# Kernel optimization log

Measured on AMD Instinct MI355X. Metric: run time of the kernel, lower is better.

Reference implementation:

```python
import jax, jax.numpy as jnp
import numpy as np
from jax import lax

B = 32768  # number of 5x5 patches processed in a batch
NUM_MID = 6  # middle 25->25 conv layers (layers 1..6 of 8)
NUM_W = 6    # predicted kernel weights per pixel


def _conv(x, w, b, pad):
    # x: [B,C,H,W], w: [O,I,kh,kw]
    y = lax.conv_general_dilated(x, w, (1, 1), pad,
                                 dimension_numbers=('NCHW', 'OIHW', 'NCHW'))
    return y + b[None, :, None, None]


def setup_inputs() -> dict:
    key = jax.random.key(0)
    ks = jax.random.split(key, 10)
    s = 0.1
    inp = {
        'input': jax.random.normal(ks[0], (B, 8, 5, 5), dtype=jnp.float32),
        'w0': jax.random.normal(ks[1], (25, 8, 3, 3), dtype=jnp.float32) * s,
        'b0': jax.random.normal(ks[2], (25,), dtype=jnp.float32) * s,
        'wmid': jax.random.normal(ks[3], (NUM_MID, 25, 25, 3, 3), dtype=jnp.float32) * s,
        'bmid': jax.random.normal(ks[4], (NUM_MID, 25), dtype=jnp.float32) * s,
        'wlast': jax.random.normal(ks[5], (NUM_W, 25, 3, 3), dtype=jnp.float32) * s,
        'blast': jax.random.normal(ks[6], (NUM_W,), dtype=jnp.float32) * s,
        'wpost': jax.random.normal(ks[7], (3 * NUM_W, 3, 5, 5), dtype=jnp.float32) * s,
        'bpost': jax.random.normal(ks[8], (3 * NUM_W,), dtype=jnp.float32) * s,
    }
    return inp


def reference(input, w0, b0, wmid, bmid, wlast, blast, wpost, bpost):
    # 8-layer tiny CNN predicting per-pixel softmax weights over NUM_W kernels
    h = jax.nn.relu(_conv(input, w0, b0, 'SAME'))
    for i in range(NUM_MID):  # fixed small layer count
        h = jax.nn.relu(_conv(h, wmid[i], bmid[i], 'SAME'))
    h = _conv(h, wlast, blast, 'SAME')            # [B, NUM_W, 5, 5]
    norm_w = jax.nn.softmax(h, axis=1)            # softmax over weight channels
    # postconv: 5x5 valid conv on first 3 channels -> [B, 3*NUM_W, 1, 1] -> [B,3,NUM_W]
    colors = _conv(input[:, 0:3], wpost, bpost, 'VALID').reshape(B, 3, NUM_W)
    # per-pixel matmul: filtered[:,y,x] = colors @ norm_w[:,y,x]
    filtered = jnp.einsum('bcw,bwyx->bcyx', colors, norm_w)  # [B,3,5,5]
    return filtered
```

## Files before the change

kernel.cpp:

```cpp
#include <hip/hip_runtime.h>
#include <hip/hip_bf16.h>
#include <stdint.h>


typedef short bf16x8 __attribute__((ext_vector_type(8)));
typedef float f32x4  __attribute__((ext_vector_type(4)));

#define WSB_N     73728
#define WSB_EMB   6144
#define WSF_BYTE  147456
#define WSF_BALL  0
#define WSF_BP32  256

#define L_STAGE_STRIDE 136
#define L_INPK   6800
#define L_COLB   12944
#define L_POOL   14096
#define SMB_STRIDE 98

__device__ __forceinline__ float b2f(unsigned short u) {
  union { unsigned int u; float f; } v; v.u = ((unsigned int)u) << 16; return v.f;
}
__device__ __forceinline__ unsigned short f2b(float f) {
  union { float f; unsigned int u; } v; v.f = f;
  unsigned int r = v.u + 0x7fffu + ((v.u >> 16) & 1u);
  return (unsigned short)(r >> 16);
}
__device__ __forceinline__ unsigned int pk2(float lo, float hi) {
  __hip_bfloat162 h = __float22bfloat162_rn(make_float2(lo, hi));
  union { __hip_bfloat162 h; unsigned int u; } v; v.h = h; return v.u;
}
__device__ __forceinline__ bool sniff_is_f32(const void* w0raw) {
  const unsigned short* q = (const unsigned short*)w0raw;
  int hits = 0;
  #pragma unroll
  for (int i = 0; i < 64; ++i) {
    unsigned int e = (q[i] >> 7) & 0xFFu;
    if (e >= 130u) ++hits;
  }
  return hits > 0;
}
__device__ __forceinline__ float ldw(const void* p, long idx, bool f32) {
  return f32 ? ((const float*)p)[idx] : b2f(((const unsigned short*)p)[idx]);
}
__device__ __forceinline__ int kperm(int m) {
  return (m < 16) ? ((m >> 2) * 8 + (m & 3))
                  : (((m - 16) >> 2) * 8 + 4 + (m & 3));
}

__global__ void prep_weights(const void* __restrict__ w0,
                             const void* __restrict__ b0,
                             const void* __restrict__ wm,
                             const void* __restrict__ bm,
                             const void* __restrict__ wl,
                             const void* __restrict__ bl,
                             const void* __restrict__ wp,
                             const void* __restrict__ bp,
                             unsigned short* __restrict__ wsb,
                             float* __restrict__ wsf) {
  const bool f32 = sniff_is_f32(w0);
  int e = blockIdx.x * blockDim.x + threadIdx.x;
  if (e < WSB_N) {
    int l = e / 9216, r = e % 9216, t = r / 1024, r2 = r % 1024;
    int o = r2 >> 5, c = r2 & 31;
    if (l == 7 && o >= 6) return;
    float v = 0.f;
    if (l < 7) {
      int co = kperm(o);
      if (co < 25) {
        if (l == 0) { if (c < 8)  v = ldw(w0, (co * 8 + c) * 9 + t, f32); }
        else        { if (c < 25) v = ldw(wm, (((l - 1) * 25 + co) * 25 + c) * 9 + t, f32); }
      }
    } else {
      if (c < 25) v = ldw(wl, (o * 25 + c) * 9 + t, f32);
    }
    wsb[e] = f2b(v);
  } else if (e < WSB_N + WSB_EMB) {
    int idx = e - WSB_N;
    int hl = idx / 3072, rem = idx % 3072;
    int chunk = rem / 1024, r2 = rem % 1024;
    int o = r2 >> 5, k = r2 & 31;
    float w = (o < 18 && k < 25) ? ldw(wp, (o * 3 + chunk) * 25 + k, f32) : 0.f;
    unsigned short hi = f2b(w);
    unsigned short val = hl ? f2b(w - b2f(hi)) : hi;
    int rowidx = hl * 96 + chunk * 32 + o;
    int t = rowidx / 26, rr = 6 + rowidx % 26;
    wsb[7 * 9216 + t * 1024 + rr * 32 + k] = val;
  } else {
    int q = e - WSB_N - WSB_EMB;
    if (q < 256) {
      int l = q >> 5, m = q & 31;
      float v = 0.f;
      if (l < 7) {
        int co = kperm(m);
        if (co < 25) v = (l == 0) ? ldw(b0, co, f32) : ldw(bm, (l - 1) * 25 + co, f32);
      } else {
        if (m < 6) v = ldw(bl, m, f32);
      }
      wsf[WSF_BALL + q] = v;
    } else if (q < 288) {
      int oc = q - 256;
      wsf[WSF_BP32 + oc] = (oc < 18) ? ldw(bp, oc, f32) : 0.f;
    }
  }
}

__global__ __launch_bounds__(64)
__attribute__((amdgpu_waves_per_eu(2, 2)))
void pcnn_mfma(
    const void* __restrict__ inp,
    const void* __restrict__ w0raw,
    const unsigned short* __restrict__ wsb,
    const float* __restrict__ wsf,
    void* __restrict__ out) {
  __shared__ __align__(16) unsigned char pool[L_POOL];
  short* stage = (short*)pool;
  short* inpk  = (short*)(pool + L_INPK);
  float* colb  = (float*)(pool + L_COLB);
  float* smb   = (float*)pool;

  const bool f32m = sniff_is_f32(w0raw);
  const int lane = threadIdx.x;
  const int col  = lane & 15;
  const int quad = lane >> 4;
  const long g   = blockIdx.x;

  bf16x8 WC[2][3][2];
  #pragma unroll
  for (int hl = 0; hl < 2; ++hl)
    #pragma unroll
    for (int ch = 0; ch < 3; ++ch)
      #pragma unroll
      for (int hf = 0; hf < 2; ++hf) {
        const int rowidx = hl * 96 + ch * 32 + hf * 16 + col;
        const int t = rowidx / 26, rr = 6 + rowidx % 26;
        WC[hl][ch][hf] = *(const bf16x8*)(wsb + 7 * 9216 + t * 1024 + rr * 32 + quad * 8);
      }
  f32x4 c0 = *(const f32x4*)(wsf + WSF_BP32 + quad * 4);
  f32x4 c1 = *(const f32x4*)(wsf + WSF_BP32 + 16 + quad * 4);

  for (int i = lane; i < 672; i += 64) {
    int s = 25 + i % 7, rest = i / 7;
    inpk[rest * 32 + s] = 0;
  }

  #pragma unroll 1
  for (int c0i = 0; c0i < 3200; c0i += 1600) {
    float v[25];
    #pragma unroll
    for (int j = 0; j < 25; ++j)
      v[j] = ldw(inp, g * 3200 + c0i + j * 64 + lane, f32m);
    #pragma unroll
    for (int j = 0; j < 25; ++j) {
      const int e = c0i + j * 64 + lane;
      int b = e / 200, r = e % 200, c = r / 25, px = r % 25;
      unsigned short hi = f2b(v[j]);
      stage[px * L_STAGE_STRIDE + b * 8 + c] = hi;
      if (c < 3) {
        inpk[((0 * 3 + c) * 16 + b) * 32 + px] = hi;
        inpk[((1 * 3 + c) * 16 + b) * 32 + px] = f2b(v[j] - b2f(hi));
      }
    }
  }
  __asm__ volatile("s_waitcnt lgkmcnt(0)" ::: "memory");

  #pragma unroll
  for (int ch = 0; ch < 3; ++ch) {
    bf16x8 Bhi = *(const bf16x8*)(inpk + ((0 * 3 + ch) * 16 + col) * 32 + quad * 8);
    bf16x8 Blo = *(const bf16x8*)(inpk + ((1 * 3 + ch) * 16 + col) * 32 + quad * 8);
    c0 = __builtin_amdgcn_mfma_f32_16x16x32_bf16(WC[0][ch][0], Bhi, c0, 0, 0, 0);
    c0 = __builtin_amdgcn_mfma_f32_16x16x32_bf16(WC[0][ch][0], Blo, c0, 0, 0, 0);
    c0 = __builtin_amdgcn_mfma_f32_16x16x32_bf16(WC[1][ch][0], Bhi, c0, 0, 0, 0);
    c1 = __builtin_amdgcn_mfma_f32_16x16x32_bf16(WC[0][ch][1], Bhi, c1, 0, 0, 0);
    c1 = __builtin_amdgcn_mfma_f32_16x16x32_bf16(WC[0][ch][1], Blo, c1, 0, 0, 0);
    c1 = __builtin_amdgcn_mfma_f32_16x16x32_bf16(WC[1][ch][1], Bhi, c1, 0, 0, 0);
  }
  #pragma unroll
  for (int r = 0; r < 4; ++r) colb[col * 18 + quad * 4 + r] = c0[r];
  if (quad == 0) { colb[col * 18 + 16] = c1[0]; colb[col * 18 + 17] = c1[1]; }

  bf16x8 X[25], Y[25];
  #pragma unroll
  for (int p = 0; p < 25; ++p) {
    union { bf16x8 v; uint4 q4; } t;
    t.q4 = make_uint4(0u, 0u, 0u, 0u);
    if (quad == 0) t.q4 = *(const uint4*)(stage + p * L_STAGE_STRIDE + col * 8);
    X[p] = t.v;
  }

  auto conv = [&](const bf16x8 (&in)[25], bf16x8 (&outp)[25], int l) {
    const unsigned short* WA = wsb + l * 9216;
    bf16x8 A0[9], A1[9];
    #pragma unroll
    for (int t = 0; t < 9; ++t) {
      A0[t] = *(const bf16x8*)(WA + t * 1024 + col * 32 + quad * 8);
      A1[t] = *(const bf16x8*)(WA + t * 1024 + (16 + col) * 32 + quad * 8);
    }
    const f32x4 bias0 = *(const f32x4*)(wsf + WSF_BALL + l * 32 + quad * 4);
    const f32x4 bias1 = *(const f32x4*)(wsf + WSF_BALL + l * 32 + 16 + quad * 4);
    f32x4 p0e, p0o, p1e, p1o;
    #pragma unroll
    for (int p = 0; p < 25; ++p) {
      const int py = p / 5, pxx = p % 5;
      f32x4 a0e = bias0, a1e = bias1;
      f32x4 a0o = {0.f, 0.f, 0.f, 0.f}, a1o = {0.f, 0.f, 0.f, 0.f};
      __builtin_amdgcn_s_setprio(1);
      #pragma unroll
      for (int dy = -1; dy <= 1; ++dy)
        #pragma unroll
        for (int dx = -1; dx <= 1; ++dx)
          if ((unsigned)(py + dy) < 5u && (unsigned)(pxx + dx) < 5u) {
            const int t = (dy + 1) * 3 + (dx + 1);
            const int q = p + dy * 5 + dx;
            if (t & 1) {
              a0o = __builtin_amdgcn_mfma_f32_16x16x32_bf16(A0[t], in[q], a0o, 0, 0, 0);
              a1o = __builtin_amdgcn_mfma_f32_16x16x32_bf16(A1[t], in[q], a1o, 0, 0, 0);
            } else {
              a0e = __builtin_amdgcn_mfma_f32_16x16x32_bf16(A0[t], in[q], a0e, 0, 0, 0);
              a1e = __builtin_amdgcn_mfma_f32_16x16x32_bf16(A1[t], in[q], a1e, 0, 0, 0);
            }
          }
      __builtin_amdgcn_s_setprio(0);
      if (p > 0) {
        union { bf16x8 v; unsigned int uu[4]; } nb;
        nb.uu[0] = pk2(fmaxf(p0e[0] + p0o[0], 0.f), fmaxf(p0e[1] + p0o[1], 0.f));
        nb.uu[1] = pk2(fmaxf(p0e[2] + p0o[2], 0.f), fmaxf(p0e[3] + p0o[3], 0.f));
        nb.uu[2] = pk2(fmaxf(p1e[0] + p1o[0], 0.f), fmaxf(p1e[1] + p1o[1], 0.f));
        nb.uu[3] = pk2(fmaxf(p1e[2] + p1o[2], 0.f), fmaxf(p1e[3] + p1o[3], 0.f));
        outp[p - 1] = nb.v;
      }
      p0e = a0e; p0o = a0o; p1e = a1e; p1o = a1o;
    }
    {
      union { bf16x8 v; unsigned int uu[4]; } nb;
      nb.uu[0] = pk2(fmaxf(p0e[0] + p0o[0], 0.f), fmaxf(p0e[1] + p0o[1], 0.f));
      nb.uu[1] = pk2(fmaxf(p0e[2] + p0o[2], 0.f), fmaxf(p0e[3] + p0o[3], 0.f));
      nb.uu[2] = pk2(fmaxf(p1e[0] + p1o[0], 0.f), fmaxf(p1e[1] + p1o[1], 0.f));
      nb.uu[3] = pk2(fmaxf(p1e[2] + p1o[2], 0.f), fmaxf(p1e[3] + p1o[3], 0.f));
      outp[24] = nb.v;
    }
  };

  conv(X, Y, 0);
  #pragma unroll 1
  for (int i = 0; i < 3; ++i) {
    conv(Y, X, 2 * i + 1);
    conv(X, Y, 2 * i + 2);
  }

  {
    const unsigned short* WA = wsb + 7 * 9216;
    bf16x8 A[9];
    #pragma unroll
    for (int t = 0; t < 9; ++t)
      A[t] = *(const bf16x8*)(WA + t * 1024 + col * 32 + quad * 8);
    const f32x4 biasl = *(const f32x4*)(wsf + WSF_BALL + 7 * 32 + quad * 4);
    f32x4 pa;
    auto tail = [&](const f32x4& a, int p) {
      float l4 = __shfl_xor(a[0], 16);
      float l5 = __shfl_xor(a[1], 16);
      if (quad == 0) {
        float m = fmaxf(fmaxf(fmaxf(a[0], a[1]), fmaxf(a[2], a[3])), fmaxf(l4, l5));
        float e0 = __expf(a[0] - m), e1 = __expf(a[1] - m), e2 = __expf(a[2] - m);
        float e3 = __expf(a[3] - m), e4 = __expf(l4 - m), e5 = __expf(l5 - m);
        float inv = 1.f / (e0 + e1 + e2 + e3 + e4 + e5);
        float* sp = smb + p * SMB_STRIDE + col * 6;
        sp[0] = e0 * inv; sp[1] = e1 * inv; sp[2] = e2 * inv;
        sp[3] = e3 * inv; sp[4] = e4 * inv; sp[5] = e5 * inv;
      }
    };
    #pragma unroll
    for (int p = 0; p < 25; ++p) {
      const int py = p / 5, pxx = p % 5;
      f32x4 ae = biasl, ao = {0.f, 0.f, 0.f, 0.f};
      __builtin_amdgcn_s_setprio(1);
      #pragma unroll
      for (int dy = -1; dy <= 1; ++dy)
        #pragma unroll
        for (int dx = -1; dx <= 1; ++dx)
          if ((unsigned)(py + dy) < 5u && (unsigned)(pxx + dx) < 5u) {
            const int t = (dy + 1) * 3 + (dx + 1);
            const int q = p + dy * 5 + dx;
            if (t & 1)
              ao = __builtin_amdgcn_mfma_f32_16x16x32_bf16(A[t], Y[q], ao, 0, 0, 0);
            else
              ae = __builtin_amdgcn_mfma_f32_16x16x32_bf16(A[t], Y[q], ae, 0, 0, 0);
          }
      __builtin_amdgcn_s_setprio(0);
      if (p > 0) tail(pa, p - 1);
      f32x4 a;
      a[0] = ae[0] + ao[0]; a[1] = ae[1] + ao[1];
      a[2] = ae[2] + ao[2]; a[3] = ae[3] + ao[3];
      pa = a;
    }
    tail(pa, 24);
  }
  __asm__ volatile("s_waitcnt lgkmcnt(0)" ::: "memory");

  for (int e = lane; e < 1200; e += 64) {
    int b = e / 75, r = e % 75, c = r / 25, p = r % 25;
    float v = 0.f;
    #pragma unroll
    for (int w = 0; w < 6; ++w)
      v = fmaf(colb[b * 18 + c * 6 + w], smb[p * SMB_STRIDE + b * 6 + w], v);
    const long oidx = g * 1200 + e;
    if (f32m) ((float*)out)[oidx] = v;
    else      ((unsigned short*)out)[oidx] = f2b(v);
  }
}

extern "C" void kernel_launch(void* const* d_in, const int* in_sizes, int n_in,
                              void* d_out, int out_size, void* d_ws, size_t ws_size,
                              hipStream_t stream) {
  unsigned short* wsb = (unsigned short*)d_ws;
  float* wsf = (float*)((char*)d_ws + WSF_BYTE);
  const int B = in_sizes[0] / 200;

  const int prep_n = WSB_N + WSB_EMB + 288;
  prep_weights<<<(prep_n + 255) / 256, 256, 0, stream>>>(
      d_in[1], d_in[2], d_in[3], d_in[4], d_in[5], d_in[6], d_in[7], d_in[8],
      wsb, wsf);
  pcnn_mfma<<<B / 16, 64, 0, stream>>>(d_in[0], d_in[1], wsb, wsf, d_out);
}
```

Measured before the change: 155.0 us.

## Pack first conv layer's 9 taps into K dimension to cut wasted MFMAs

The first layer has only 8 input channels, so each 32-wide K slot of an MFMA was mostly zeros. Layer 0 weights are now repacked so four taps share one K=32 slice, which brings the layer down to at most three MFMA groups per pixel. Each lane loads its tap-shifted input straight from the LDS staging buffer, and a new zero row at index 25 serves out-of-bounds taps. This adds per-pixel address arithmetic and LDS reads, and the LDS layout offsets grow to make room for the padding row.

```diff
diff --git a/kernel.cpp b/kernel.cpp
--- a/kernel.cpp
+++ b/kernel.cpp
@@ -13,9 +13,9 @@
 #define WSF_BP32  256
 
 #define L_STAGE_STRIDE 136
-#define L_INPK   6800
-#define L_COLB   12944
-#define L_POOL   14096
+#define L_INPK   7072
+#define L_COLB   13216
+#define L_POOL   14368
 #define SMB_STRIDE 98
 
 __device__ __forceinline__ float b2f(unsigned short u) {
@@ -65,12 +65,16 @@
     int o = r2 >> 5, c = r2 & 31;
     if (l == 7 && o >= 6) return;
     float v = 0.f;
-    if (l < 7) {
+    if (l == 0) {
       int co = kperm(o);
-      if (co < 25) {
-        if (l == 0) { if (c < 8)  v = ldw(w0, (co * 8 + c) * 9 + t, f32); }
-        else        { if (c < 25) v = ldw(wm, (((l - 1) * 25 + co) * 25 + c) * 9 + t, f32); }
-      }
+      if (t < 3 && co < 25) {
+        int tq = c >> 3, j = c & 7, tap = t * 4 + tq;
+        if (tap < 9) v = ldw(w0, (co * 8 + j) * 9 + tap, f32);
+      }
+    } else if (l < 7) {
+      int co = kperm(o);
+      if (co < 25 && c < 25)
+        v = ldw(wm, (((l - 1) * 25 + co) * 25 + c) * 9 + t, f32);
     } else {
       if (c < 25) v = ldw(wl, (o * 25 + c) * 9 + t, f32);
     }
@@ -143,6 +147,8 @@
     int s = 25 + i % 7, rest = i / 7;
     inpk[rest * 32 + s] = 0;
   }
+  for (int i = lane; i < L_STAGE_STRIDE; i += 64)
+    stage[25 * L_STAGE_STRIDE + i] = 0;
 
   #pragma unroll 1
   for (int c0i = 0; c0i < 3200; c0i += 1600) {
@@ -180,12 +186,90 @@
   if (quad == 0) { colb[col * 18 + 16] = c1[0]; colb[col * 18 + 17] = c1[1]; }
 
   bf16x8 X[25], Y[25];
-  #pragma unroll
-  for (int p = 0; p < 25; ++p) {
-    union { bf16x8 v; uint4 q4; } t;
-    t.q4 = make_uint4(0u, 0u, 0u, 0u);
-    if (quad == 0) t.q4 = *(const uint4*)(stage + p * L_STAGE_STRIDE + col * 8);
-    X[p] = t.v;
+
+  {
+    const unsigned short* WA = wsb;
+    bf16x8 G0[3], G1[3];
+    #pragma unroll
+    for (int gq = 0; gq < 3; ++gq) {
+      G0[gq] = *(const bf16x8*)(WA + gq * 1024 + col * 32 + quad * 8);
+      G1[gq] = *(const bf16x8*)(WA + gq * 1024 + (16 + col) * 32 + quad * 8);
+    }
+    const f32x4 bias0 = *(const f32x4*)(wsf + WSF_BALL + quad * 4);
+    const f32x4 bias1 = *(const f32x4*)(wsf + WSF_BALL + 16 + quad * 4);
+    int tdy[3], tdx[3], tvl[3];
+    #pragma unroll
+    for (int gq = 0; gq < 3; ++gq) {
+      int tap = gq * 4 + quad;
+      tvl[gq] = (tap < 9) ? 1 : 0;
+      tdy[gq] = tap / 3 - 1;
+      tdx[gq] = tap % 3 - 1;
+    }
+    auto bload = [&](int p, int gq) -> bf16x8 {
+      int py = p / 5, pxx = p % 5;
+      bool ok = tvl[gq] && ((unsigned)(py + tdy[gq]) < 5u) &&
+                ((unsigned)(pxx + tdx[gq]) < 5u);
+      int q = ok ? (p + tdy[gq] * 5 + tdx[gq]) : 25;
+      return *(const bf16x8*)(stage + q * L_STAGE_STRIDE + col * 8);
+    };
+    auto gne = [](int p, int gq) -> bool {
+      int py = p / 5, pxx = p % 5;
+      for (int tq = 0; tq < 4; ++tq) {
+        int tap = gq * 4 + tq;
+        if (tap < 9) {
+          int dy = tap / 3 - 1, dx = tap % 3 - 1;
+          if ((unsigned)(py + dy) < 5u && (unsigned)(pxx + dx) < 5u) return true;
+        }
+      }
+      return false;
+    };
+    f32x4 p0e, p0o, p1e, p1o;
+    bf16x8 Bc0, Bc1, Bc2, Bn0, Bn1, Bn2;
+    if (gne(0, 0)) Bc0 = bload(0, 0);
+    if (gne(0, 1)) Bc1 = bload(0, 1);
+    if (gne(0, 2)) Bc2 = bload(0, 2);
+    #pragma unroll
+    for (int p = 0; p < 25; ++p) {
+      if (p < 24) {
+        if (gne(p + 1, 0)) Bn0 = bload(p + 1, 0);
+        if (gne(p + 1, 1)) Bn1 = bload(p + 1, 1);
+        if (gne(p + 1, 2)) Bn2 = bload(p + 1, 2);
+      }
+      f32x4 a0e = bias0, a1e = bias1;
+      f32x4 a0o = {0.f, 0.f, 0.f, 0.f}, a1o = {0.f, 0.f, 0.f, 0.f};
+      __builtin_amdgcn_s_setprio(1);
+      if (gne(p, 0)) {
+        a0e = __builtin_amdgcn_mfma_f32_16x16x32_bf16(G0[0], Bc0, a0e, 0, 0, 0);
+        a1e = __builtin_amdgcn_mfma_f32_16x16x32_bf16(G1[0], Bc0, a1e, 0, 0, 0);
+      }
+      if (gne(p, 1)) {
+        a0o = __builtin_amdgcn_mfma_f32_16x16x32_bf16(G0[1], Bc1, a0o, 0, 0, 0);
+        a1o = __builtin_amdgcn_mfma_f32_16x16x32_bf16(G1[1], Bc1, a1o, 0, 0, 0);
+      }
+      if (gne(p, 2)) {
+        a0e = __builtin_amdgcn_mfma_f32_16x16x32_bf16(G0[2], Bc2, a0e, 0, 0, 0);
+        a1e = __builtin_amdgcn_mfma_f32_16x16x32_bf16(G1[2], Bc2, a1e, 0, 0, 0);
+      }
+      __builtin_amdgcn_s_setprio(0);
+      if (p > 0) {
+        union { bf16x8 v; unsigned int uu[4]; } nb;
+        nb.uu[0] = pk2(fmaxf(p0e[0] + p0o[0], 0.f), fmaxf(p0e[1] + p0o[1], 0.f));
+        nb.uu[1] = pk2(fmaxf(p0e[2] + p0o[2], 0.f), fmaxf(p0e[3] + p0o[3], 0.f));
+        nb.uu[2] = pk2(fmaxf(p1e[0] + p1o[0], 0.f), fmaxf(p1e[1] + p1o[1], 0.f));
+        nb.uu[3] = pk2(fmaxf(p1e[2] + p1o[2], 0.f), fmaxf(p1e[3] + p1o[3], 0.f));
+        Y[p - 1] = nb.v;
+      }
+      p0e = a0e; p0o = a0o; p1e = a1e; p1o = a1o;
+      Bc0 = Bn0; Bc1 = Bn1; Bc2 = Bn2;
+    }
+    {
+      union { bf16x8 v; unsigned int uu[4]; } nb;
+      nb.uu[0] = pk2(fmaxf(p0e[0] + p0o[0], 0.f), fmaxf(p0e[1] + p0o[1], 0.f));
+      nb.uu[1] = pk2(fmaxf(p0e[2] + p0o[2], 0.f), fmaxf(p0e[3] + p0o[3], 0.f));
+      nb.uu[2] = pk2(fmaxf(p1e[0] + p1o[0], 0.f), fmaxf(p1e[1] + p1o[1], 0.f));
+      nb.uu[3] = pk2(fmaxf(p1e[2] + p1o[2], 0.f), fmaxf(p1e[3] + p1o[3], 0.f));
+      Y[24] = nb.v;
+    }
   }
 
   auto conv = [&](const bf16x8 (&in)[25], bf16x8 (&outp)[25], int l) {
@@ -241,7 +325,6 @@
     }
   };
 
-  conv(X, Y, 0);
   #pragma unroll 1
   for (int i = 0; i < 3; ++i) {
     conv(Y, X, 2 * i + 1);
```

Result: slower. 176.5 us (+13.9%).
